# Kernel tuning notes

Hardware: AMD Instinct MI355X
Metric: run time of the kernel (lower is better)

## Reference

```python
import jax, jax.numpy as jnp
import numpy as np

B, A, D, H = 32, 64, 128, 512
F = A * D  # 8192

def setup_inputs() -> dict:
    key = jax.random.key(0)
    ks = jax.random.split(key, 20)
    s = 0.02
    return {
        "swarm_states": jax.random.normal(ks[0], (B, A, D), jnp.float32),
        "swarm_goals": jax.random.normal(ks[1], (B, A, D), jnp.float32),
        # quantum layer stand-in: Linear(F->F) + tanh
        "Wq": jax.random.normal(ks[2], (F, F), jnp.float32) * s,
        "bq": jnp.zeros((F,), jnp.float32),
        # interaction_net: Linear(2D->H) ReLU Linear(H->H) ReLU Linear(H->D)
        "Wi1": jax.random.normal(ks[3], (2 * D, H), jnp.float32) * s,
        "bi1": jnp.zeros((H,), jnp.float32),
        "Wi2": jax.random.normal(ks[4], (H, H), jnp.float32) * s,
        "bi2": jnp.zeros((H,), jnp.float32),
        "Wi3": jax.random.normal(ks[5], (H, D), jnp.float32) * s,
        "bi3": jnp.zeros((D,), jnp.float32),
        # coordination_net: Linear(F->H) ReLU Linear(H->H) ReLU Linear(H->F)
        "Wc1": jax.random.normal(ks[6], (F, H), jnp.float32) * s,
        "bc1": jnp.zeros((H,), jnp.float32),
        "Wc2": jax.random.normal(ks[7], (H, H), jnp.float32) * s,
        "bc2": jnp.zeros((H,), jnp.float32),
        "Wc3": jax.random.normal(ks[8], (H, F), jnp.float32) * s,
        "bc3": jnp.zeros((F,), jnp.float32),
    }

def reference(swarm_states, swarm_goals, Wq, bq, Wi1, bi1, Wi2, bi2, Wi3, bi3,
              Wc1, bc1, Wc2, bc2, Wc3, bc3):
    b, a, d = swarm_states.shape
    states_flat = swarm_states.reshape(b, a * d)
    # quantum feature extraction (stand-in for QuantumNeuralLayer)
    quantum_features = jnp.tanh(states_flat @ Wq + bq)  # (B, A*D)

    # vectorized pairwise interaction MLP over all ordered (i, j) pairs
    xi = jnp.broadcast_to(swarm_states[:, :, None, :], (b, a, a, d))
    xj = jnp.broadcast_to(swarm_states[:, None, :, :], (b, a, a, d))
    pair = jnp.concatenate([xi, xj], axis=-1)            # (B, A, A, 2D)
    h = jax.nn.relu(pair @ Wi1 + bi1)
    h = jax.nn.relu(h @ Wi2 + bi2)
    inter = h @ Wi3 + bi3                                # (B, A, A, D)
    offdiag = (1.0 - jnp.eye(a, dtype=inter.dtype))[None, :, :, None]
    # per-agent aggregation over the other agents (mean over j != i)
    interactions = (inter * offdiag).sum(axis=2) / (a - 1)  # (B, A, D)

    c = jax.nn.relu(quantum_features @ Wc1 + bc1)
    c = jax.nn.relu(c @ Wc2 + bc2)
    coordination = (c @ Wc3 + bc3).reshape(b, a, d)      # (B, A, D)

    coordinated_states = swarm_states + 0.1 * interactions + 0.1 * coordination
    return coordinated_states, quantum_features, interactions, coordination
```

## Files before the change

### kernel.cpp

```cpp
#include <hip/hip_runtime.h>

typedef __attribute__((ext_vector_type(8))) short bf16x8;
typedef __attribute__((ext_vector_type(16))) float f32x16;
typedef _Float16 f16;
typedef __attribute__((ext_vector_type(8))) _Float16 f16x8;

static __device__ __forceinline__ unsigned short f2bf(float x) {
  unsigned int u = __float_as_uint(x);
  return (unsigned short)((u + 0x7FFFu + ((u >> 16) & 1u)) >> 16);
}
static __device__ __forceinline__ unsigned int pk2bf(float lo, float hi) {
  return ((unsigned int)f2bf(hi) << 16) | f2bf(lo);
}
static __device__ __forceinline__ f16x8 relu8(f16x8 x) {
  f16x8 z = {0, 0, 0, 0, 0, 0, 0, 0};
  return __builtin_elementwise_max(x, z);
}

__global__ __launch_bounds__(256) void prep_kernel(const float* __restrict__ states,
                                                   const float* __restrict__ Wi2,
                                                   const float* __restrict__ Wi1,
                                                   const float* __restrict__ bi1,
                                                   unsigned short* __restrict__ Sbf,
                                                   f16* __restrict__ W2h,
                                                   f16* __restrict__ Uh, f16* __restrict__ Vh) {
  __shared__ float lds_f[1536];
  const int t = threadIdx.x;
  const int bid = blockIdx.x;
  if (bid < 256) {
    const int idx = bid * 256 + t;
    float4 v = ((const float4*)states)[idx];
    ushort4 o;
    o.x = f2bf(v.x); o.y = f2bf(v.y); o.z = f2bf(v.z); o.w = f2bf(v.w);
    ((ushort4*)Sbf)[idx] = o;
  } else if (bid < 512) {
    const int b = bid - 256;
    const int bk = b & 15, bn = b >> 4;
    float (*tile)[33] = (float(*)[33])lds_f;
    const int r = t >> 5, c = t & 31;
#pragma unroll
    for (int p = 0; p < 4; p++) {
      int rr = p * 8 + r;
      tile[rr][c] = Wi2[(bk * 32 + rr) * 512 + bn * 32 + c];
    }
    __syncthreads();
#pragma unroll
    for (int p = 0; p < 4; p++) {
      int rr = p * 8 + r;
      W2h[(bn * 32 + rr) * 512 + bk * 32 + c] = (f16)tile[c][rr];
    }
  } else {
    const int row0 = (bid - 512) * 8;
    float (*st)[12] = (float(*)[12])lds_f;
    for (int idx = t; idx < 1024; idx += 256) {
      int r = idx >> 7, k = idx & 127;
      st[k][r] = states[(row0 + r) * 128 + k];
    }
    __syncthreads();
    float au0[8], au1[8], av0[8], av1[8];
#pragma unroll
    for (int r = 0; r < 8; r++) { au0[r] = 0.f; au1[r] = 0.f; av0[r] = 0.f; av1[r] = 0.f; }
#pragma unroll 4
    for (int k = 0; k < 128; k++) {
      float wt0 = Wi1[k * 512 + t];
      float wt1 = Wi1[k * 512 + 256 + t];
      float wb0 = Wi1[(k + 128) * 512 + t];
      float wb1 = Wi1[(k + 128) * 512 + 256 + t];
      float4 sA = *(const float4*)&st[k][0];
      float4 sB = *(const float4*)&st[k][4];
      float s8[8] = {sA.x, sA.y, sA.z, sA.w, sB.x, sB.y, sB.z, sB.w};
#pragma unroll
      for (int r = 0; r < 8; r++) {
        au0[r] += s8[r] * wt0;
        au1[r] += s8[r] * wt1;
        av0[r] += s8[r] * wb0;
        av1[r] += s8[r] * wb1;
      }
    }
    const float b0 = bi1[t], b1 = bi1[256 + t];
#pragma unroll
    for (int r = 0; r < 8; r++) {
      Uh[(row0 + r) * 512 + t]       = (f16)(au0[r] + b0);
      Uh[(row0 + r) * 512 + 256 + t] = (f16)(au1[r] + b1);
      Vh[(row0 + r) * 512 + t]       = (f16)av0[r];
      Vh[(row0 + r) * 512 + 256 + t] = (f16)av1[r];
    }
  }
}

__global__ __launch_bounds__(256, 4) void gemmw(const unsigned short* __restrict__ Abf,
                                                const float* __restrict__ W,
                                                float* __restrict__ P,
                                                int K, int N, int L, int l4sh) {
  __shared__ __align__(16) unsigned short As[32 * 512];
  const int t = threadIdx.x;
  const int k0 = blockIdx.y * L;
  const int L4 = L >> 2;
  const int swzm = 2 * L - 1;
  for (int idx = t; idx < (L << 3); idx += 256) {
    int row = idx >> l4sh, k4 = idx & (L4 - 1);
    ushort4 a4 = *(const ushort4*)&Abf[(size_t)row * K + k0 + k4 * 4];
    int off = (row * 2 * L + k4 * 8) ^ (((row & 7) << 4) & swzm);
    *(ushort4*)((char*)As + off) = a4;
  }
  __syncthreads();
  const int lane = t & 63, w = t >> 6;
  const int lrow = lane & 31, lh = lane >> 5;
  const int col = blockIdx.x * 128 + w * 32 + lrow;
  f32x16 acc0, acc1;
#pragma unroll
  for (int r = 0; r < 16; r++) { acc0[r] = 0.f; acc1[r] = 0.f; }
  const float* Wp = W + (size_t)(k0 + lh * 8) * N + col;
  const int aswz = ((lrow & 7) << 4) & swzm;
  const int abase = lrow * 2 * L + lh * 16;
  const int nks = L >> 4;
  int ks = 0;
  for (; ks + 1 < nks; ks += 2) {
    float wv0[8], wv1[8];
#pragma unroll
    for (int jj = 0; jj < 8; jj++) wv0[jj] = Wp[(size_t)(ks * 16 + jj) * N];
#pragma unroll
    for (int jj = 0; jj < 8; jj++) wv1[jj] = Wp[(size_t)(ks * 16 + 16 + jj) * N];
    uint4 b0, b1;
    b0.x = pk2bf(wv0[0], wv0[1]); b0.y = pk2bf(wv0[2], wv0[3]);
    b0.z = pk2bf(wv0[4], wv0[5]); b0.w = pk2bf(wv0[6], wv0[7]);
    b1.x = pk2bf(wv1[0], wv1[1]); b1.y = pk2bf(wv1[2], wv1[3]);
    b1.z = pk2bf(wv1[4], wv1[5]); b1.w = pk2bf(wv1[6], wv1[7]);
    bf16x8 af0 = *(const bf16x8*)((const char*)As + ((abase + ks * 32) ^ aswz));
    bf16x8 af1 = *(const bf16x8*)((const char*)As + ((abase + ks * 32 + 32) ^ aswz));
    acc0 = __builtin_amdgcn_mfma_f32_32x32x16_bf16(af0, *(const bf16x8*)&b0, acc0, 0, 0, 0);
    acc1 = __builtin_amdgcn_mfma_f32_32x32x16_bf16(af1, *(const bf16x8*)&b1, acc1, 0, 0, 0);
  }
  if (ks < nks) {
    float wv0[8];
#pragma unroll
    for (int jj = 0; jj < 8; jj++) wv0[jj] = Wp[(size_t)(ks * 16 + jj) * N];
    uint4 b0;
    b0.x = pk2bf(wv0[0], wv0[1]); b0.y = pk2bf(wv0[2], wv0[3]);
    b0.z = pk2bf(wv0[4], wv0[5]); b0.w = pk2bf(wv0[6], wv0[7]);
    bf16x8 af0 = *(const bf16x8*)((const char*)As + ((abase + ks * 32) ^ aswz));
    acc0 = __builtin_amdgcn_mfma_f32_32x32x16_bf16(af0, *(const bf16x8*)&b0, acc0, 0, 0, 0);
  }
  float* Pr = P + (size_t)blockIdx.y * 32 * N + col;
#pragma unroll
  for (int r = 0; r < 16; r++) {
    int row = (r & 3) + 8 * (r >> 2) + 4 * lh;
    Pr[(size_t)row * N] = acc0[r] + acc1[r];
  }
}

__global__ __launch_bounds__(256) void reduce_kernel(const float* __restrict__ P,
                                                     const float* __restrict__ bias,
                                                     float* __restrict__ dst,
                                                     unsigned short* __restrict__ dstbf,
                                                     int lnN, int KS, int act, int wbf,
                                                     const float* __restrict__ S,
                                                     const float* __restrict__ Ip,
                                                     float* __restrict__ out0, int comb) {
  const int idx = blockIdx.x * 256 + threadIdx.x;
  const int N = 1 << lnN;
  const int m = idx >> lnN, n = idx & (N - 1);
  float s = 0.f;
#pragma unroll 8
  for (int p = 0; p < KS; p++) s += P[((size_t)(p * 32 + m) << lnN) + n];
  s += bias[n];
  if (act == 1) s = fmaxf(s, 0.f);
  else if (act == 2) s = tanhf(s);
  dst[idx] = s;
  if (wbf) dstbf[idx] = f2bf(s);
  if (comb) out0[idx] = S[idx] + 0.1f * (Ip[idx] + s);
}

__global__ __launch_bounds__(512, 2) void inter6_kernel(const f16* __restrict__ Uh,
                                                        const f16* __restrict__ Vh,
                                                        const f16* __restrict__ W2h,
                                                        const float* __restrict__ bi2,
                                                        float* __restrict__ Hsum) {
  __shared__ __align__(16) f16 Bt[128 * 512];
  __shared__ __align__(16) f16 Vc[64 * 128];
  const int t = threadIdx.x;
  const int nq = blockIdx.x;

#pragma unroll
  for (int i = 0; i < 16; i++) {
    int idx = i * 512 + t;
    int n = idx >> 6, ch = idx & 63;
    f16x8 w8 = *(const f16x8*)&W2h[(size_t)(nq * 128 + n) * 512 + ch * 8];
    int off = (n * 1024 + ch * 16) ^ ((n & 15) << 4);
    *(f16x8*)((char*)Bt + off) = w8;
  }

  const int w = t >> 6, lane = t & 63;
  const int ii = w & 1, tg = w >> 1;
  const int lrow = lane & 31, lh = lane >> 5;
  const char* Btc = (const char*)Bt;
  const char* Vcc = (const char*)Vc;
  char* Vcw = (char*)Vc;

  int bofs[4], bswz[4];
#pragma unroll
  for (int nf = 0; nf < 4; nf++) {
    int nr = nf * 32 + lrow;
    bofs[nf] = nr * 1024 + lh * 16;
    bswz[nf] = (nr & 15) << 4;
  }
  const int vofs0 = lrow * 256;
  const int vswz0 = (lrow & 15) << 4;
  const int vofs1 = (lrow + 32) * 256;
  const int vswz1 = vswz0;

  const int b = blockIdx.y >> 1;

  for (int s = 0; s < 4; s++) {
    const int tid = blockIdx.y * 16 + tg * 4 + s;
    const int it = tid & 31;
    const f16* Ub = Uh + (size_t)(b * 64 + it * 2 + ii) * 512 + lh * 8;

    f32x16 acc[2][4];
#pragma unroll
    for (int mf = 0; mf < 2; mf++)
#pragma unroll
      for (int nf = 0; nf < 4; nf++)
#pragma unroll
        for (int r = 0; r < 16; r++) acc[mf][nf][r] = 0.f;

    for (int ch = 0; ch < 4; ch++) {
      const int kc = ch * 128;
      __syncthreads();
#pragma unroll
      for (int i = 0; i < 2; i++) {
        int idx = i * 512 + t;
        int row = idx >> 4, c8 = idx & 15;
        f16x8 w8 = *(const f16x8*)&Vh[(size_t)(b * 64 + row) * 512 + kc + c8 * 8];
        *(f16x8*)(Vcw + ((row * 256 + c8 * 16) ^ ((row & 15) << 4))) = w8;
      }
      __syncthreads();
#pragma unroll
      for (int k16 = 0; k16 < 8; k16++) {
        const int kb2 = k16 * 32 + lh * 16;
        f16x8 v0 = *(const f16x8*)(Vcc + ((vofs0 + kb2) ^ vswz0));
        f16x8 v1 = *(const f16x8*)(Vcc + ((vofs1 + kb2) ^ vswz1));
        f16x8 u0 = *(const f16x8*)(Ub + kc + k16 * 16);
        f16x8 a0 = relu8(v0 + u0);
        f16x8 a1 = relu8(v1 + u0);
#pragma unroll
        for (int nf = 0; nf < 4; nf++) {
          f16x8 bfr = *(const f16x8*)(Btc + ((bofs[nf] + (kc + k16 * 16) * 2) ^ bswz[nf]));
          acc[0][nf] = __builtin_amdgcn_mfma_f32_32x32x16_f16(a0, bfr, acc[0][nf], 0, 0, 0);
          acc[1][nf] = __builtin_amdgcn_mfma_f32_32x32x16_f16(a1, bfr, acc[1][nf], 0, 0, 0);
        }
      }
    }

    const int iglob = it * 2 + ii;
    const int mf_d = iglob >> 5;
    const int rd = iglob & 31;
    const int lh_d = (rd >> 2) & 1;
    const int r_d = (rd & 3) + 4 * (rd >> 3);
#pragma unroll
    for (int nf = 0; nf < 4; nf++) {
      const int col = nq * 128 + nf * 32 + lrow;
      const float b2 = bi2[col];
      float ssum = 0.f;
#pragma unroll
      for (int mf = 0; mf < 2; mf++)
#pragma unroll
        for (int r = 0; r < 16; r++) {
          float x = fmaxf(acc[mf][nf][r] + b2, 0.f);
          if (mf == mf_d && r == r_d && lh == lh_d) x = 0.f;
          ssum += x;
        }
      ssum += __shfl_xor(ssum, 32);
      if (lh == 0) Hsum[(size_t)(b * 64 + iglob) * 512 + col] = ssum;
    }
  }
}

__global__ __launch_bounds__(256) void k3_kernel(const float* __restrict__ Hsum,
                                                 const float* __restrict__ Wi3,
                                                 const float* __restrict__ bi3,
                                                 float* __restrict__ inter) {
  __shared__ float st[512][10];
  const int t = threadIdx.x;
  const int row0 = blockIdx.x * 8;
  for (int idx = t; idx < 4096; idx += 256) {
    int r = idx >> 9, k = idx & 511;
    st[k][r] = Hsum[(row0 + r) * 512 + k] * (1.0f / 63.0f);
  }
  __syncthreads();
  const int c = t & 63;
  const int rg = t >> 6;
  float a0[2] = {0.f, 0.f}, a1[2] = {0.f, 0.f};
#pragma unroll 4
  for (int k = 0; k < 512; k++) {
    float w0 = Wi3[k * 128 + c];
    float w1 = Wi3[k * 128 + 64 + c];
    float2 h = *(const float2*)&st[k][rg * 2];
    a0[0] += h.x * w0; a0[1] += h.y * w0;
    a1[0] += h.x * w1; a1[1] += h.y * w1;
  }
  float b0 = bi3[c], b1 = bi3[64 + c];
#pragma unroll
  for (int r = 0; r < 2; r++) {
    inter[(row0 + rg * 2 + r) * 128 + c]      = a0[r] + b0;
    inter[(row0 + rg * 2 + r) * 128 + 64 + c] = a1[r] + b1;
  }
}

extern "C" void kernel_launch(void* const* d_in, const int* in_sizes, int n_in,
                              void* d_out, int out_size, void* d_ws, size_t ws_size,
                              hipStream_t stream) {
  const float* states = (const float*)d_in[0];
  const float* Wq  = (const float*)d_in[2];
  const float* bq  = (const float*)d_in[3];
  const float* Wi1 = (const float*)d_in[4];
  const float* bi1 = (const float*)d_in[5];
  const float* Wi2 = (const float*)d_in[6];
  const float* bi2 = (const float*)d_in[7];
  const float* Wi3 = (const float*)d_in[8];
  const float* bi3 = (const float*)d_in[9];
  const float* Wc1 = (const float*)d_in[10];
  const float* bc1 = (const float*)d_in[11];
  const float* Wc2 = (const float*)d_in[12];
  const float* bc2 = (const float*)d_in[13];
  const float* Wc3 = (const float*)d_in[14];
  const float* bc3 = (const float*)d_in[15];

  float* out   = (float*)d_out;
  float* out0  = out;
  float* qf    = out + 262144;
  float* inter = out + 524288;
  float* coord = out + 786432;

  char* ws = (char*)d_ws;
  float*          P    = (float*)(ws);
  f16*            Uh   = (f16*)(ws + ((size_t)16 << 20));
  f16*            Vh   = (f16*)(ws + ((size_t)19 << 20));
  f16*            W2h  = (f16*)(ws + ((size_t)22 << 20));
  float*          Hsum = (float*)(ws + ((size_t)23 << 20));
  unsigned short* Sbf  = (unsigned short*)(ws + ((size_t)27 << 20));
  unsigned short* qfbf = (unsigned short*)(ws + ((size_t)28 << 20));
  float*          c1   = (float*)(ws + ((size_t)29 << 20));
  float*          c2   = (float*)(ws + ((size_t)29 << 20) + (1 << 16));
  unsigned short* c1bf = (unsigned short*)(ws + ((size_t)29 << 20) + (2 << 16));
  unsigned short* c2bf = (unsigned short*)(ws + ((size_t)29 << 20) + (3 << 16));

  prep_kernel<<<768, 256, 0, stream>>>(states, Wi2, Wi1, bi1, Sbf, W2h, Uh, Vh);

  gemmw<<<dim3(64, 16), 256, 0, stream>>>(Sbf, Wq, P, 8192, 8192, 512, 7);
  reduce_kernel<<<1024, 256, 0, stream>>>(P, bq, qf, qfbf, 13, 16, 2, 1,
                                          nullptr, nullptr, nullptr, 0);

  inter6_kernel<<<dim3(4, 64), 512, 0, stream>>>(Uh, Vh, W2h, bi2, Hsum);
  k3_kernel<<<256, 256, 0, stream>>>(Hsum, Wi3, bi3, inter);

  gemmw<<<dim3(4, 64), 256, 0, stream>>>(qfbf, Wc1, P, 8192, 512, 128, 5);
  reduce_kernel<<<64, 256, 0, stream>>>(P, bc1, c1, c1bf, 9, 64, 1, 1,
                                        nullptr, nullptr, nullptr, 0);
  gemmw<<<dim3(4, 32), 256, 0, stream>>>(c1bf, Wc2, P, 512, 512, 16, 2);
  reduce_kernel<<<64, 256, 0, stream>>>(P, bc2, c2, c2bf, 9, 32, 1, 1,
                                        nullptr, nullptr, nullptr, 0);

  gemmw<<<dim3(64, 8), 256, 0, stream>>>(c2bf, Wc3, P, 512, 8192, 64, 4);
  reduce_kernel<<<1024, 256, 0, stream>>>(P, bc3, coord, nullptr, 13, 8, 0, 0,
                                          states, inter, out0, 1);
}
```

Before: 219.7 us.

## Add wider-column split-K GEMM kernel for the Wq projection

Adds a new kernel gemmw2 for the big 8192x8192 quantum projection. Each block covers 512 output columns and a K-slice of 256, using 32 K-splits instead of 16. Each wave computes 128 columns with four MFMA accumulators that share one A fragment, staging converted bf16 weights through a per-wave swizzled LDS scratch. The workspace layout is shifted so the partial buffer can hold 32 splits, and the reduce kernel is told to sum 32 partials. This trades more partial-sum traffic and reduction work for more blocks and higher A-fragment reuse during the weight-streaming GEMM.

```diff
diff --git a/kernel.cpp b/kernel.cpp
--- a/kernel.cpp
+++ b/kernel.cpp
@@ -88,6 +88,72 @@
   }
 }
 
+__global__ __launch_bounds__(256, 2) void gemmw2(const unsigned short* __restrict__ Abf,
+                                                 const float* __restrict__ W,
+                                                 float* __restrict__ P,
+                                                 int K, int N) {
+  __shared__ __align__(16) unsigned short As[32 * 256];
+  __shared__ __align__(16) char Xc[16384];
+  const int t = threadIdx.x;
+  const int k0 = blockIdx.y * 256;
+  for (int idx = t; idx < 2048; idx += 256) {
+    int row = idx >> 6, k4 = idx & 63;
+    ushort4 a4 = *(const ushort4*)&Abf[(size_t)row * K + k0 + k4 * 4];
+    int off = (row * 512 + k4 * 8) ^ ((row & 7) << 4);
+    *(ushort4*)((char*)As + off) = a4;
+  }
+  __syncthreads();
+
+  const int lane = t & 63, w = t >> 6;
+  const int lrow = lane & 31, lh = lane >> 5;
+  const int c0 = blockIdx.x * 512 + w * 128;
+  const float* Wb = W + (size_t)(k0 + lh * 8) * N + c0 + 4 * lrow;
+  char* wsb = Xc + w * 4096 + lh * 2048;
+  const int wslot = ((lrow & 3) ^ ((lrow >> 2) & 3)) << 4;
+  const int aswz = (lrow & 7) << 4;
+  const int abase = lrow * 512 + lh * 16;
+
+  f32x16 acc0, acc1, acc2, acc3;
+#pragma unroll
+  for (int r = 0; r < 16; r++) { acc0[r] = 0.f; acc1[r] = 0.f; acc2[r] = 0.f; acc3[r] = 0.f; }
+
+#pragma unroll 2
+  for (int kt = 0; kt < 16; kt++) {
+    float vr[8][4];
+#pragma unroll
+    for (int j = 0; j < 8; j++)
+      *(float4*)&vr[j][0] = *(const float4*)&Wb[(size_t)(kt * 16 + j) * N];
+#pragma unroll
+    for (int i = 0; i < 4; i++) {
+      uint4 b;
+      b.x = pk2bf(vr[0][i], vr[1][i]);
+      b.y = pk2bf(vr[2][i], vr[3][i]);
+      b.z = pk2bf(vr[4][i], vr[5][i]);
+      b.w = pk2bf(vr[6][i], vr[7][i]);
+      *(uint4*)(wsb + lrow * 64 + (((i ^ (lrow & 3)) << 4))) = b;
+    }
+    bf16x8 af = *(const bf16x8*)((const char*)As + ((abase + kt * 32) ^ aswz));
+    bf16x8 bf0 = *(const bf16x8*)(wsb + ((lrow >> 2) + 0)  * 64 + wslot);
+    bf16x8 bf1 = *(const bf16x8*)(wsb + ((lrow >> 2) + 8)  * 64 + wslot);
+    bf16x8 bf2 = *(const bf16x8*)(wsb + ((lrow >> 2) + 16) * 64 + wslot);
+    bf16x8 bf3 = *(const bf16x8*)(wsb + ((lrow >> 2) + 24) * 64 + wslot);
+    acc0 = __builtin_amdgcn_mfma_f32_32x32x16_bf16(af, bf0, acc0, 0, 0, 0);
+    acc1 = __builtin_amdgcn_mfma_f32_32x32x16_bf16(af, bf1, acc1, 0, 0, 0);
+    acc2 = __builtin_amdgcn_mfma_f32_32x32x16_bf16(af, bf2, acc2, 0, 0, 0);
+    acc3 = __builtin_amdgcn_mfma_f32_32x32x16_bf16(af, bf3, acc3, 0, 0, 0);
+  }
+
+  float* Pr = P + (size_t)blockIdx.y * 32 * N + c0;
+#pragma unroll
+  for (int r = 0; r < 16; r++) {
+    int row = (r & 3) + 8 * (r >> 2) + 4 * lh;
+    Pr[(size_t)row * N + lrow]      = acc0[r];
+    Pr[(size_t)row * N + 32 + lrow] = acc1[r];
+    Pr[(size_t)row * N + 64 + lrow] = acc2[r];
+    Pr[(size_t)row * N + 96 + lrow] = acc3[r];
+  }
+}
+
 __global__ __launch_bounds__(256, 4) void gemmw(const unsigned short* __restrict__ Abf,
                                                 const float* __restrict__ W,
                                                 float* __restrict__ P,
@@ -334,21 +400,21 @@
 
   char* ws = (char*)d_ws;
   float*          P    = (float*)(ws);
-  f16*            Uh   = (f16*)(ws + ((size_t)16 << 20));
-  f16*            Vh   = (f16*)(ws + ((size_t)19 << 20));
-  f16*            W2h  = (f16*)(ws + ((size_t)22 << 20));
-  float*          Hsum = (float*)(ws + ((size_t)23 << 20));
-  unsigned short* Sbf  = (unsigned short*)(ws + ((size_t)27 << 20));
-  unsigned short* qfbf = (unsigned short*)(ws + ((size_t)28 << 20));
-  float*          c1   = (float*)(ws + ((size_t)29 << 20));
-  float*          c2   = (float*)(ws + ((size_t)29 << 20) + (1 << 16));
-  unsigned short* c1bf = (unsigned short*)(ws + ((size_t)29 << 20) + (2 << 16));
-  unsigned short* c2bf = (unsigned short*)(ws + ((size_t)29 << 20) + (3 << 16));
+  f16*            Uh   = (f16*)(ws + ((size_t)33 << 20));
+  f16*            Vh   = (f16*)(ws + ((size_t)36 << 20));
+  f16*            W2h  = (f16*)(ws + ((size_t)39 << 20));
+  float*          Hsum = (float*)(ws + ((size_t)40 << 20));
+  unsigned short* Sbf  = (unsigned short*)(ws + ((size_t)44 << 20));
+  unsigned short* qfbf = (unsigned short*)(ws + ((size_t)45 << 20));
+  float*          c1   = (float*)(ws + ((size_t)46 << 20));
+  float*          c2   = (float*)(ws + ((size_t)46 << 20) + (1 << 16));
+  unsigned short* c1bf = (unsigned short*)(ws + ((size_t)46 << 20) + (2 << 16));
+  unsigned short* c2bf = (unsigned short*)(ws + ((size_t)46 << 20) + (3 << 16));
 
   prep_kernel<<<768, 256, 0, stream>>>(states, Wi2, Wi1, bi1, Sbf, W2h, Uh, Vh);
 
-  gemmw<<<dim3(64, 16), 256, 0, stream>>>(Sbf, Wq, P, 8192, 8192, 512, 7);
-  reduce_kernel<<<1024, 256, 0, stream>>>(P, bq, qf, qfbf, 13, 16, 2, 1,
+  gemmw2<<<dim3(16, 32), 256, 0, stream>>>(Sbf, Wq, P, 8192, 8192);
+  reduce_kernel<<<1024, 256, 0, stream>>>(P, bq, qf, qfbf, 13, 32, 2, 1,
                                           nullptr, nullptr, nullptr, 0);
 
   inter6_kernel<<<dim3(4, 64), 512, 0, stream>>>(Uh, Vh, W2h, bi2, Hsum);
```

After: 251.2 us. +14.3%, slower.
